# Kernel tuning notes

Measured on AMD Instinct MI355X. Metric: run time of the kernel, lower is better.

The kernel has to match this reference:

```python
import jax, jax.numpy as jnp
import numpy as np

BN_EPS = 1e-5


def setup_inputs() -> dict:
    key = jax.random.key(0)
    ks = jax.random.split(key, 8)
    B, S, D, H, O = 4, 25000, 128, 128, 128
    N, E = B * S, 600000
    x = jax.random.normal(ks[0], (B, S, D), dtype=jnp.float32)
    edge_index = jax.random.randint(ks[1], (2, E), 0, N)
    W1 = jax.random.normal(ks[2], (D, H), dtype=jnp.float32) * (1.0 / np.sqrt(D))
    b1 = jnp.zeros((H,), jnp.float32)
    gamma1 = jnp.ones((H,), jnp.float32)
    beta1 = jnp.zeros((H,), jnp.float32)
    W2 = jax.random.normal(ks[3], (H, O), dtype=jnp.float32) * (1.0 / np.sqrt(H))
    b2 = jnp.zeros((O,), jnp.float32)
    return {"x": x, "edge_index": edge_index, "W1": W1, "b1": b1,
            "gamma1": gamma1, "beta1": beta1, "W2": W2, "b2": b2}


def _gcn_norm(edge_index, num_nodes, dtype):
    # PyG gcn_norm: add self-loops, symmetric D^-1/2 (A+I) D^-1/2 edge weights.
    row, col = edge_index
    loop = jnp.arange(num_nodes, dtype=row.dtype)
    row_f = jnp.concatenate([row, loop])
    col_f = jnp.concatenate([col, loop])
    deg = jax.ops.segment_sum(jnp.ones(row_f.shape, dtype), row_f,
                              num_segments=num_nodes)
    dis = jnp.where(deg > 0, jax.lax.rsqrt(jnp.maximum(deg, 1e-12)), 0.0)
    norm = dis[row_f] * dis[col_f]  # [E + N]
    return row_f, col_f, norm


def _gcn_conv(h, W, b, row_f, col_f, norm, num_nodes):
    hw = h @ W                       # [N, out]
    msg = hw[col_f] * norm[:, None]  # gather + scale, [E+N, out]
    out = jax.ops.segment_sum(msg, row_f, num_segments=num_nodes)
    return out + b


def reference(x, edge_index, W1, b1, gamma1, beta1, W2, b2):
    B, S, D = x.shape
    N = B * S
    h = x.reshape(N, D)
    row_f, col_f, norm = _gcn_norm(edge_index, N, h.dtype)
    # layer 1: GCNConv -> BatchNorm (batch stats) -> ReLU (dropout inactive in eval)
    h = _gcn_conv(h, W1, b1, row_f, col_f, norm, N)
    mean = jnp.mean(h, axis=0)
    var = jnp.mean(jnp.square(h - mean), axis=0)
    h = gamma1 * (h - mean) * jax.lax.rsqrt(var + BN_EPS) + beta1
    h = jax.nn.relu(h)
    # layer 2: final GCNConv
    h = _gcn_conv(h, W2, b2, row_f, col_f, norm, N)
    return h.reshape(B, S, -1)
```

## Files before the change

### kernel.cpp

```cpp
#include <hip/hip_runtime.h>

#define DIM 128
#define BN_EPS 1e-5f
#define STAT_COPIES 64

typedef short short8 __attribute__((ext_vector_type(8)));
typedef float floatx4 __attribute__((ext_vector_type(4)));

__device__ __forceinline__ unsigned short f2bf(float f) {
    unsigned int u = __builtin_bit_cast(unsigned int, f);
    u += 0x7FFFu + ((u >> 16) & 1u);
    return (unsigned short)(u >> 16);
}
__device__ __forceinline__ float bf2f(unsigned short h) {
    return __builtin_bit_cast(float, (unsigned int)h << 16);
}


__global__ __launch_bounds__(256) void deg_convw_kernel(
    const int* __restrict__ row, int* __restrict__ deg, int E, int degB,
    const float* __restrict__ W1, const float* __restrict__ W2,
    unsigned short* __restrict__ wfrag)
{
    if ((int)blockIdx.x < degB) {
        int e = blockIdx.x * 256 + threadIdx.x;
        if (e < E) atomicAdd(&deg[row[e]], 1);
    } else {
        int s = (blockIdx.x - degB) * 256 + threadIdx.x;
        if (s >= 4096) return;
        int m  = s >> 11;
        int s2 = s & 2047;
        int kt = s2 >> 9;
        int nt = (s2 >> 6) & 7;
        int l  = s2 & 63;
        const float* W = m ? W2 : W1;
        unsigned short* o = wfrag + (size_t)m * 16384 + (size_t)s2 * 8;
        int k0 = kt * 32 + (l >> 4) * 8;
        int n0 = nt * 16 + (l & 15);
        #pragma unroll
        for (int j = 0; j < 8; ++j) o[j] = f2bf(W[(k0 + j) * DIM + n0]);
    }
}


__global__ __launch_bounds__(256) void scan_block_kernel(const int* __restrict__ deg,
                                                         int* __restrict__ rowptr,
                                                         int* __restrict__ aux,
                                                         float* __restrict__ dis, int n) {
    __shared__ int ls[256];
    const int base = blockIdx.x * 1024;
    const int t = threadIdx.x;
    int v[4]; int s = 0;
    #pragma unroll
    for (int k = 0; k < 4; ++k) {
        int i = base + t * 4 + k;
        v[k] = (i < n) ? deg[i] : 0;
        s += v[k];
    }
    ls[t] = s;
    __syncthreads();
    for (int off = 1; off < 256; off <<= 1) {
        int x = (t >= off) ? ls[t - off] : 0;
        __syncthreads();
        ls[t] += x;
        __syncthreads();
    }
    int excl = ls[t] - s;
    if (t == 255) aux[blockIdx.x] = ls[255];
    #pragma unroll
    for (int k = 0; k < 4; ++k) {
        int i = base + t * 4 + k;
        if (i < n) {
            rowptr[i] = excl;
            dis[i] = rsqrtf((float)(v[k] + 1));
        }
        excl += v[k];
    }
}


__global__ __launch_bounds__(256) void add_offsets_kernel(
    const int* __restrict__ rowptr, const int* __restrict__ deg,
    const int* __restrict__ aux, int2* __restrict__ rp2,
    int* __restrict__ cursor, int n)
{
    __shared__ int red[256];
    const int t = threadIdx.x;
    red[t] = (t < (int)blockIdx.x) ? aux[t] : 0;
    __syncthreads();
    for (int off = 128; off > 0; off >>= 1) {
        if (t < off) red[t] += red[t + off];
        __syncthreads();
    }
    const int base = red[0];
    #pragma unroll
    for (int k = 0; k < 4; ++k) {
        int i = blockIdx.x * 1024 + t * 4 + k;
        if (i < n) {
            int st = rowptr[i] + base;
            rp2[i] = make_int2(st, st + deg[i]);
            cursor[i] = st;
        }
    }
}


__global__ __launch_bounds__(256) void scatter_gemm1_kernel(
    const int* __restrict__ row, const int* __restrict__ col,
    const float* __restrict__ dis, int* __restrict__ cursor,
    int2* __restrict__ epack, int E, int scatB,
    const float* __restrict__ A, const unsigned short* __restrict__ wfrag,
    unsigned short* __restrict__ C, int n)
{
    if ((int)blockIdx.x < scatB) {
        int e = blockIdx.x * 256 + threadIdx.x;
        if (e >= E) return;
        int r = row[e], c = col[e];
        int pos = atomicAdd(&cursor[r], 1);
        float nrm = dis[r] * dis[c];
        epack[pos] = make_int2(c, __builtin_bit_cast(int, nrm));
    } else {
        __shared__ unsigned short sA[64][136];
        const int tid  = threadIdx.x;
        const int row0 = (blockIdx.x - scatB) * 64;

        #pragma unroll
        for (int l = 0; l < 8; ++l) {
            int idx = tid + l * 256;
            int r   = idx >> 5;
            int c4  = (idx & 31) * 4;
            float4 v;
            if (row0 + r < n) v = *(const float4*)(A + (size_t)(row0 + r) * DIM + c4);
            else              v = make_float4(0.f, 0.f, 0.f, 0.f);
            unsigned int lo = (unsigned int)f2bf(v.x) | ((unsigned int)f2bf(v.y) << 16);
            unsigned int hi = (unsigned int)f2bf(v.z) | ((unsigned int)f2bf(v.w) << 16);
            *(uint2*)(&sA[r][c4]) = make_uint2(lo, hi);
        }
        __syncthreads();

        const int wave = tid >> 6;
        const int lane = tid & 63;
        const int m    = lane & 15;
        const int quad = lane >> 4;
        const int rowA = wave * 16 + m;

        short8 af[4];
        #pragma unroll
        for (int kt = 0; kt < 4; ++kt)
            af[kt] = *(const short8*)(&sA[rowA][kt * 32 + quad * 8]);

        floatx4 acc[8];
        #pragma unroll
        for (int nt = 0; nt < 8; ++nt) acc[nt] = (floatx4){0.f, 0.f, 0.f, 0.f};

        #pragma unroll
        for (int nt = 0; nt < 8; ++nt)
            #pragma unroll
            for (int kt = 0; kt < 4; ++kt) {
                short8 bfr = *(const short8*)(wfrag + ((size_t)(kt * 8 + nt) * 64 + lane) * 8);
                acc[nt] = __builtin_amdgcn_mfma_f32_16x16x32_bf16(af[kt], bfr, acc[nt], 0, 0, 0);
            }

        #pragma unroll
        for (int nt = 0; nt < 8; ++nt)
            #pragma unroll
            for (int r = 0; r < 4; ++r) {
                int rr = row0 + wave * 16 + quad * 4 + r;
                if (rr < n) C[(size_t)rr * DIM + nt * 16 + m] = f2bf(acc[nt][r]);
            }
    }
}


__global__ __launch_bounds__(256) void gemm_mfma_bn_kernel(
    const unsigned short* __restrict__ A, const unsigned short* __restrict__ wfrag,
    unsigned short* __restrict__ C, int n,
    const float* __restrict__ mi)
{
    __shared__ unsigned short sA[64][136];
    const int tid  = threadIdx.x;
    const int row0 = blockIdx.x * 64;

    #pragma unroll
    for (int l = 0; l < 4; ++l) {
        int idx = tid + l * 256;
        int r   = idx >> 4;
        int c8  = (idx & 15) * 8;
        uint4 u = make_uint4(0, 0, 0, 0);
        if (row0 + r < n) u = *(const uint4*)(A + (size_t)(row0 + r) * DIM + c8);
        float f[8] = { bf2f((unsigned short)(u.x & 0xffff)), bf2f((unsigned short)(u.x >> 16)),
                       bf2f((unsigned short)(u.y & 0xffff)), bf2f((unsigned short)(u.y >> 16)),
                       bf2f((unsigned short)(u.z & 0xffff)), bf2f((unsigned short)(u.z >> 16)),
                       bf2f((unsigned short)(u.w & 0xffff)), bf2f((unsigned short)(u.w >> 16)) };
        #pragma unroll
        for (int k = 0; k < 8; ++k) {
            int c = c8 + k;
            f[k] = fmaxf(fmaf(f[k], mi[c], mi[128 + c]), 0.f);
        }
        uint4 o;
        o.x = (unsigned int)f2bf(f[0]) | ((unsigned int)f2bf(f[1]) << 16);
        o.y = (unsigned int)f2bf(f[2]) | ((unsigned int)f2bf(f[3]) << 16);
        o.z = (unsigned int)f2bf(f[4]) | ((unsigned int)f2bf(f[5]) << 16);
        o.w = (unsigned int)f2bf(f[6]) | ((unsigned int)f2bf(f[7]) << 16);
        *(uint4*)(&sA[r][c8]) = o;
    }
    __syncthreads();

    const int wave = tid >> 6;
    const int lane = tid & 63;
    const int m    = lane & 15;
    const int quad = lane >> 4;
    const int rowA = wave * 16 + m;

    short8 af[4];
    #pragma unroll
    for (int kt = 0; kt < 4; ++kt)
        af[kt] = *(const short8*)(&sA[rowA][kt * 32 + quad * 8]);

    floatx4 acc[8];
    #pragma unroll
    for (int nt = 0; nt < 8; ++nt) acc[nt] = (floatx4){0.f, 0.f, 0.f, 0.f};

    #pragma unroll
    for (int nt = 0; nt < 8; ++nt)
        #pragma unroll
        for (int kt = 0; kt < 4; ++kt) {
            short8 bfr = *(const short8*)(wfrag + ((size_t)(kt * 8 + nt) * 64 + lane) * 8);
            acc[nt] = __builtin_amdgcn_mfma_f32_16x16x32_bf16(af[kt], bfr, acc[nt], 0, 0, 0);
        }

    #pragma unroll
    for (int nt = 0; nt < 8; ++nt)
        #pragma unroll
        for (int r = 0; r < 4; ++r) {
            int rr = row0 + wave * 16 + quad * 4 + r;
            if (rr < n) C[(size_t)rr * DIM + nt * 16 + m] = f2bf(acc[nt][r]);
        }
}


__device__ __forceinline__ void acc8(float* acc, uint4 u, float w) {
    unsigned int a[4] = {u.x, u.y, u.z, u.w};
    #pragma unroll
    for (int k = 0; k < 4; ++k) {
        acc[2*k]   = fmaf(bf2f((unsigned short)(a[k] & 0xffff)), w, acc[2*k]);
        acc[2*k+1] = fmaf(bf2f((unsigned short)(a[k] >> 16)),    w, acc[2*k+1]);
    }
}

template <bool OUT_BF16, bool STATS>
__global__ __launch_bounds__(256) void agg_csr_kernel(
    const unsigned short* __restrict__ hw, const float* __restrict__ dis,
    const int2* __restrict__ rp2, const int2* __restrict__ epack,
    const float* __restrict__ bias, void* __restrict__ out_, int n,
    float* __restrict__ stat)
{
    const int sub  = threadIdx.x >> 4;
    const int l    = threadIdx.x & 15;
    const int node = blockIdx.x * 16 + sub;
    const bool valid = node < n;
    const int j = l * 8;

    float acc[8];
    #pragma unroll
    for (int k = 0; k < 8; ++k) acc[k] = 0.f;

    if (valid) {
        const int2 rp = rp2[node];
        {
            const float d = dis[node];
            uint4 u = *(const uint4*)(hw + (size_t)node * DIM + j);
            acc8(acc, u, d * d);
        }

        const int pe = rp.y;
        for (int p = rp.x; p < pe; p += 8) {
            const int pm = pe - 1;
            int2 e[8];
            #pragma unroll
            for (int k = 0; k < 8; ++k) {
                int pk = p + k;
                e[k] = epack[pk < pm ? pk : pm];
            }
            uint4 u[8];
            #pragma unroll
            for (int k = 0; k < 8; ++k)
                u[k] = *(const uint4*)(hw + (size_t)e[k].x * DIM + j);
            #pragma unroll
            for (int k = 0; k < 8; ++k) {
                float w = (p + k < pe) ? __builtin_bit_cast(float, e[k].y) : 0.f;
                acc8(acc, u[k], w);
            }
        }

        float4 b0 = *(const float4*)(bias + j);
        float4 b1 = *(const float4*)(bias + j + 4);
        acc[0] += b0.x; acc[1] += b0.y; acc[2] += b0.z; acc[3] += b0.w;
        acc[4] += b1.x; acc[5] += b1.y; acc[6] += b1.z; acc[7] += b1.w;

        if (OUT_BF16) {
            unsigned short* out = (unsigned short*)out_;
            uint4 o;
            o.x = (unsigned int)f2bf(acc[0]) | ((unsigned int)f2bf(acc[1]) << 16);
            o.y = (unsigned int)f2bf(acc[2]) | ((unsigned int)f2bf(acc[3]) << 16);
            o.z = (unsigned int)f2bf(acc[4]) | ((unsigned int)f2bf(acc[5]) << 16);
            o.w = (unsigned int)f2bf(acc[6]) | ((unsigned int)f2bf(acc[7]) << 16);
            *(uint4*)(out + (size_t)node * DIM + j) = o;
        } else {
            float* out = (float*)out_;
            *(float4*)(out + (size_t)node * DIM + j)     = make_float4(acc[0], acc[1], acc[2], acc[3]);
            *(float4*)(out + (size_t)node * DIM + j + 4) = make_float4(acc[4], acc[5], acc[6], acc[7]);
        }
    }

    if constexpr (STATS) {
        __shared__ float red[16][257];
        #pragma unroll
        for (int k = 0; k < 8; ++k) {
            float a = valid ? acc[k] : 0.f;
            red[sub][j + k]       = a;
            red[sub][128 + j + k] = a * a;
        }
        __syncthreads();
        float t = 0.f;
        #pragma unroll
        for (int r = 0; r < 16; ++r) t += red[r][threadIdx.x];
        atomicAdd(&stat[(blockIdx.x & (STAT_COPIES - 1)) * 256 + threadIdx.x], t);
    }
}


__global__ void bn_finalize_kernel(const float* __restrict__ stat,
                                   const float* __restrict__ gamma,
                                   const float* __restrict__ beta,
                                   float* __restrict__ mi, int n) {
    int c = threadIdx.x;
    if (c < DIM) {
        float s = 0.f, q = 0.f;
        #pragma unroll 4
        for (int cp = 0; cp < STAT_COPIES; ++cp) {
            s += stat[cp * 256 + c];
            q += stat[cp * 256 + 128 + c];
        }
        float mean  = s / (float)n;
        float var   = q / (float)n - mean * mean;
        float istd  = rsqrtf(var + BN_EPS);
        float scale = gamma[c] * istd;
        mi[c]       = scale;
        mi[DIM + c] = fmaf(-mean, scale, beta[c]);
    }
}


extern "C" void kernel_launch(void* const* d_in, const int* in_sizes, int n_in,
                              void* d_out, int out_size, void* d_ws, size_t ws_size,
                              hipStream_t stream)
{
    const float* x      = (const float*)d_in[0];
    const int*   ei     = (const int*)  d_in[1];
    const float* W1     = (const float*)d_in[2];
    const float* b1     = (const float*)d_in[3];
    const float* gamma1 = (const float*)d_in[4];
    const float* beta1  = (const float*)d_in[5];
    const float* W2     = (const float*)d_in[6];
    const float* b2     = (const float*)d_in[7];
    float* out = (float*)d_out;

    const int N = in_sizes[0] / DIM;
    const int E = in_sizes[1] / 2;
    const int* row = ei;
    const int* col = ei + E;

    const int NB    = (N + 1023) / 1024;
    const int degB  = (E + 255) / 256;
    const int gemmB = (N + 63) / 64;
    const int aggB  = (N + 15) / 16;

    unsigned short* hw    = (unsigned short*)d_ws;
    unsigned short* h1    = hw + (size_t)N * DIM;
    int2*  epack  = (int2*)(h1 + (size_t)N * DIM);
    int2*  rp2    = epack + E;
    unsigned short* wfrag = (unsigned short*)(rp2 + N);
    float* dis    = (float*)(wfrag + 2 * 16384);
    int*   cursor = (int*)(dis + N);
    int*   rowptr = cursor + N;
    int*   aux    = rowptr + N;
    float* mi     = (float*)(aux + 256);
    int*   deg    = (int*)(mi + 256);
    float* stat   = (float*)(deg + N);
    const size_t zero_bytes = (size_t)N * 4 + (size_t)STAT_COPIES * 256 * 4;

    hipMemsetAsync(deg, 0, zero_bytes, stream);

    deg_convw_kernel<<<degB + 16, 256, 0, stream>>>(row, deg, E, degB, W1, W2, wfrag);
    scan_block_kernel<<<NB, 256, 0, stream>>>(deg, rowptr, aux, dis, N);
    add_offsets_kernel<<<NB, 256, 0, stream>>>(rowptr, deg, aux, rp2, cursor, N);
    scatter_gemm1_kernel<<<degB + gemmB, 256, 0, stream>>>(row, col, dis, cursor, epack,
                                                           E, degB, x, wfrag, hw, N);
    agg_csr_kernel<true, true><<<aggB, 256, 0, stream>>>(hw, dis, rp2, epack, b1, h1, N,
                                                         stat);
    bn_finalize_kernel<<<1, DIM, 0, stream>>>(stat, gamma1, beta1, mi, N);
    gemm_mfma_bn_kernel<<<gemmB, 256, 0, stream>>>(h1, wfrag + 16384, hw, N, mi);
    agg_csr_kernel<false, false><<<aggB, 256, 0, stream>>>(hw, dis, rp2, epack, b2, out, N,
                                                           nullptr);
}
```

Measured before the change: 273.5 us.

## Record edge rank during degree count and interleave scatter with GEMM blocks

The degree-counting kernel now saves the value returned by each atomic increment as the edge's rank within its row. The scatter phase then computes the CSR position as rowptr plus rank, which removes the second round of atomics on a cursor array. The fused scatter/GEMM kernel also interleaves its blocks (3 scatter blocks to 2 GEMM blocks) so memory-bound and compute-bound work share the GPU at the same time. The cost is an extra E-sized rank array that is written once and read once.

```diff
diff --git a/kernel.cpp b/kernel.cpp
--- a/kernel.cpp
+++ b/kernel.cpp
@@ -18,13 +18,14 @@
 
 
 __global__ __launch_bounds__(256) void deg_convw_kernel(
-    const int* __restrict__ row, int* __restrict__ deg, int E, int degB,
+    const int* __restrict__ row, int* __restrict__ deg, int* __restrict__ rank,
+    int E, int degB,
     const float* __restrict__ W1, const float* __restrict__ W2,
     unsigned short* __restrict__ wfrag)
 {
     if ((int)blockIdx.x < degB) {
         int e = blockIdx.x * 256 + threadIdx.x;
-        if (e < E) atomicAdd(&deg[row[e]], 1);
+        if (e < E) rank[e] = atomicAdd(&deg[row[e]], 1);
     } else {
         int s = (blockIdx.x - degB) * 256 + threadIdx.x;
         if (s >= 4096) return;
@@ -81,8 +82,7 @@
 
 __global__ __launch_bounds__(256) void add_offsets_kernel(
     const int* __restrict__ rowptr, const int* __restrict__ deg,
-    const int* __restrict__ aux, int2* __restrict__ rp2,
-    int* __restrict__ cursor, int n)
+    const int* __restrict__ aux, int2* __restrict__ rp2, int n)
 {
     __shared__ int red[256];
     const int t = threadIdx.x;
@@ -99,7 +99,6 @@
         if (i < n) {
             int st = rowptr[i] + base;
             rp2[i] = make_int2(st, st + deg[i]);
-            cursor[i] = st;
         }
     }
 }
@@ -107,22 +106,28 @@
 
 __global__ __launch_bounds__(256) void scatter_gemm1_kernel(
     const int* __restrict__ row, const int* __restrict__ col,
-    const float* __restrict__ dis, int* __restrict__ cursor,
-    int2* __restrict__ epack, int E, int scatB,
+    const int* __restrict__ rank, const float* __restrict__ dis,
+    const int2* __restrict__ rp2, int2* __restrict__ epack, int E, int scatS,
     const float* __restrict__ A, const unsigned short* __restrict__ wfrag,
-    unsigned short* __restrict__ C, int n)
-{
-    if ((int)blockIdx.x < scatB) {
-        int e = blockIdx.x * 256 + threadIdx.x;
+    unsigned short* __restrict__ C, int n, int gemmG)
+{
+    const int grp = blockIdx.x / 5;
+    const int off = blockIdx.x % 5;
+    if (off < 3) {
+        const int sId = grp * 3 + off;
+        if (sId >= scatS) return;
+        int e = sId * 256 + threadIdx.x;
         if (e >= E) return;
         int r = row[e], c = col[e];
-        int pos = atomicAdd(&cursor[r], 1);
+        int pos = rp2[r].x + rank[e];
         float nrm = dis[r] * dis[c];
         epack[pos] = make_int2(c, __builtin_bit_cast(int, nrm));
     } else {
+        const int gId = grp * 2 + (off - 3);
+        if (gId >= gemmG) return;
         __shared__ unsigned short sA[64][136];
         const int tid  = threadIdx.x;
-        const int row0 = (blockIdx.x - scatB) * 64;
+        const int row0 = gId * 64;
 
         #pragma unroll
         for (int l = 0; l < 8; ++l) {
@@ -375,6 +380,7 @@
     const int degB  = (E + 255) / 256;
     const int gemmB = (N + 63) / 64;
     const int aggB  = (N + 15) / 16;
+    const int k4B   = 5 * max((degB + 2) / 3, (gemmB + 1) / 2);
 
     unsigned short* hw    = (unsigned short*)d_ws;
     unsigned short* h1    = hw + (size_t)N * DIM;
@@ -382,8 +388,8 @@
     int2*  rp2    = epack + E;
     unsigned short* wfrag = (unsigned short*)(rp2 + N);
     float* dis    = (float*)(wfrag + 2 * 16384);
-    int*   cursor = (int*)(dis + N);
-    int*   rowptr = cursor + N;
+    int*   rank   = (int*)(dis + N);
+    int*   rowptr = rank + E;
     int*   aux    = rowptr + N;
     float* mi     = (float*)(aux + 256);
     int*   deg    = (int*)(mi + 256);
@@ -392,11 +398,11 @@
 
     hipMemsetAsync(deg, 0, zero_bytes, stream);
 
-    deg_convw_kernel<<<degB + 16, 256, 0, stream>>>(row, deg, E, degB, W1, W2, wfrag);
+    deg_convw_kernel<<<degB + 16, 256, 0, stream>>>(row, deg, rank, E, degB, W1, W2, wfrag);
     scan_block_kernel<<<NB, 256, 0, stream>>>(deg, rowptr, aux, dis, N);
-    add_offsets_kernel<<<NB, 256, 0, stream>>>(rowptr, deg, aux, rp2, cursor, N);
-    scatter_gemm1_kernel<<<degB + gemmB, 256, 0, stream>>>(row, col, dis, cursor, epack,
-                                                           E, degB, x, wfrag, hw, N);
+    add_offsets_kernel<<<NB, 256, 0, stream>>>(rowptr, deg, aux, rp2, N);
+    scatter_gemm1_kernel<<<k4B, 256, 0, stream>>>(row, col, rank, dis, rp2, epack, E, degB,
+                                                  x, wfrag, hw, N, gemmB);
     agg_csr_kernel<true, true><<<aggB, 256, 0, stream>>>(hw, dis, rp2, epack, b1, h1, N,
                                                          stat);
     bn_finalize_kernel<<<1, DIM, 0, stream>>>(stat, gamma1, beta1, mi, N);
```

Measured after the change: 262.7 us. 1.04x faster.
